# Kernel tuning notes

Measured on AMD Instinct MI355X. Metric: run time of the kernel, lower is better.

## Reference

```python
import jax, jax.numpy as jnp
import numpy as np

M = 28            # mask head resolution (mask_logit[i] is MxM)
NUM_CLASSES = 80  # max value of cls_idx (mask_image channel count)


def setup_inputs() -> dict:
    key = jax.random.key(0)
    k1, k2, k3, k4, k5, k6, k7 = jax.random.split(key, 7)
    N, H, W = 100, 800, 800
    cx = jax.random.uniform(k1, (N,), minval=0.0, maxval=float(W - 1))
    cy = jax.random.uniform(k2, (N,), minval=0.0, maxval=float(H - 1))
    bw = jax.random.uniform(k3, (N,), minval=20.0, maxval=300.0)
    bh = jax.random.uniform(k4, (N,), minval=20.0, maxval=300.0)
    mask_rois = jnp.stack([cx - bw / 2, cy - bh / 2, cx + bw / 2, cy + bh / 2], axis=1).astype(jnp.float32)
    cls_prob = jax.random.uniform(k5, (N,), dtype=jnp.float32)
    mask_prob = jax.random.normal(k6, (N, M, M), dtype=jnp.float32)
    cls_idx = jax.random.randint(k7, (N,), 1, NUM_CLASSES + 1, dtype=jnp.int32)
    return {"mask_rois": mask_rois, "cls_prob": cls_prob, "mask_prob": mask_prob,
            "cls_idx": cls_idx, "im_h": H, "im_w": W}


def _paste(logit, box, H, W):
    """Bilinear-paste an MxM logit into the full HxW image (== cv2.resize to (w,h)
    then placing at the box, evaluated directly on image pixel coords)."""
    x0, y0, x1, y1 = box[0], box[1], box[2], box[3]  # int32
    w = jnp.maximum(x1 - x0 + 1, 1).astype(jnp.float32)
    h = jnp.maximum(y1 - y0 + 1, 1).astype(jnp.float32)
    xs = jnp.arange(W, dtype=jnp.float32)
    ys = jnp.arange(H, dtype=jnp.float32)
    # cv2 bilinear mapping: src = (dst + 0.5) * (M / size) - 0.5, clamped at borders
    sx = jnp.clip((xs - x0.astype(jnp.float32) + 0.5) * (M / w) - 0.5, 0.0, M - 1.0)
    sy = jnp.clip((ys - y0.astype(jnp.float32) + 0.5) * (M / h) - 0.5, 0.0, M - 1.0)
    ix0 = jnp.floor(sx).astype(jnp.int32); ix1 = jnp.minimum(ix0 + 1, M - 1); fx = sx - ix0
    iy0 = jnp.floor(sy).astype(jnp.int32); iy1 = jnp.minimum(iy0 + 1, M - 1); fy = sy - iy0
    v00 = logit[iy0[:, None], ix0[None, :]]
    v01 = logit[iy0[:, None], ix1[None, :]]
    v10 = logit[iy1[:, None], ix0[None, :]]
    v11 = logit[iy1[:, None], ix1[None, :]]
    val = ((1 - fy)[:, None] * ((1 - fx)[None, :] * v00 + fx[None, :] * v01)
           + fy[:, None] * ((1 - fx)[None, :] * v10 + fx[None, :] * v11))
    xi = jnp.arange(W, dtype=jnp.int32)
    yi = jnp.arange(H, dtype=jnp.int32)
    inside_x = (xi >= jnp.maximum(x0, 0)) & (xi < jnp.minimum(x1 + 1, W))
    inside_y = (yi >= jnp.maximum(y0, 0)) & (yi < jnp.minimum(y1 + 1, H))
    inside = inside_y[:, None] & inside_x[None, :]
    return jnp.where(inside, val, 0.0), inside


def _forward(mask_rois, cls_prob, mask_prob, cls_idx, H, W, thr):
    N = mask_prob.shape[0]
    order = jnp.argsort(-cls_prob)                       # sort by score, descending
    boxes = mask_rois[order].astype(jnp.int32)
    logits = mask_prob[order]
    cls = cls_idx[order].astype(jnp.int32) - 1           # 0-based class ids
    pasted, inside = jax.vmap(lambda l, b: _paste(l, b, H, W))(logits, boxes)  # [N,H,W]

    def step(mask_image, xs):
        logit, ins, c = xs
        mask = (logit > 0) & ins                          # thresholded, in-image crop mask
        prev = mask_image[c]
        msum = jnp.sum(mask).astype(jnp.float32)
        ovl = jnp.sum(mask & prev).astype(jnp.float32)    # overlap with accumulated class mask
        keep = (msum > 0) & (ovl <= thr * msum)           # skip if ratio > threshold
        mask_image = mask_image.at[c].set(prev | (mask & keep))
        return mask_image, keep

    mask_image0 = jnp.zeros((NUM_CLASSES, H, W), dtype=bool)
    _, keep = jax.lax.scan(step, mask_image0, (pasted, inside, cls))

    # compact kept masks to the front (frame_id order); dropped boxes go to slot N (discarded)
    pos = jnp.where(keep, jnp.cumsum(keep.astype(jnp.int32)) - 1, N)
    energy = jnp.where(inside & keep[:, None, None], pasted, 0.0)
    full = jnp.zeros((N + 1, H, W), pasted.dtype).at[pos].set(energy)
    mask_energy = full[:N][None]                          # [1, N, H, W], kept masks first
    keep_inds = jnp.full((N + 1,), -1, jnp.int32).at[pos].set(
        jnp.where(keep, order.astype(jnp.int32), -1))[:N]
    return keep_inds, mask_energy


def reference(mask_rois, cls_prob, mask_prob, cls_idx, im_h, im_w):
    return _forward(mask_rois, cls_prob, mask_prob, cls_idx, int(im_h), int(im_w), 0.3)
```

## Files before the change

### kernel.cpp

```cpp
#include <hip/hip_runtime.h>

#define NINST 100
#define MLOG 28
#define IMG 800
#define LOGSZ (MLOG * MLOG)

#define OFF_ORDER 0
#define OFF_CLS   100
#define OFF_BOX   200
#define OFF_MSUM  600
#define OFF_SLOT  800
#define OFF_NK    900
#define OFF_NPAIR 901
#define OFF_FLAG  904
#define OFF_MASK  1024
#define ROWW      12
#define MSTRIDE   (ROWW * 304)
#define OFF_PAIRS (OFF_MASK + NINST * MSTRIDE)
#define PAIR_CAP  512
#define SLOTSZ    (IMG * IMG)
#define SUBB      40
#define ROWSPB    (IMG / SUBB)
#define MEGAGRID  (1 + NINST * SUBB)

__global__ __launch_bounds__(256) void k_raster(const float* __restrict__ mask_prob,
                                                const float* __restrict__ cls_prob,
                                                const float* __restrict__ rois,
                                                const int* __restrict__ cls_idx,
                                                int* __restrict__ ws) {
    int b = blockIdx.x, tid = threadIdx.x;
    __shared__ float s_p[NINST];
    __shared__ int s_order[NINST];
    __shared__ float lg[LOGSZ];
    __shared__ int red[256];
    if (tid < NINST) s_p[tid] = cls_prob[tid];
    __syncthreads();
    if (tid < NINST) {
        float p = s_p[tid];
        int r = 0;
        for (int j = 0; j < NINST; j++) {
            float q = s_p[j];
            r += (q > p) || (q == p && j < tid);
        }
        s_order[r] = tid;
    }
    __syncthreads();
    int n = b;
    int orig = s_order[n];
    int x0 = (int)rois[4 * orig], y0 = (int)rois[4 * orig + 1];
    int x1 = (int)rois[4 * orig + 2], y1 = (int)rois[4 * orig + 3];
    if (b == 0) {
        if (tid < NINST) {
            int o = s_order[tid];
            ws[OFF_ORDER + tid] = o;
            ws[OFF_CLS + tid] = cls_idx[o] - 1;
#pragma unroll
            for (int k = 0; k < 4; k++)
                ws[OFF_BOX + 4 * tid + k] = (int)rois[4 * o + k];
        }
    }
    for (int i = tid; i < LOGSZ; i += 256) lg[i] = mask_prob[orig * LOGSZ + i];
    __syncthreads();
    int xs = max(x0, 0), xe = min(x1 + 1, IMG);
    int ys = max(y0, 0), ye = min(y1 + 1, IMG);
    int wx0 = xs >> 5, nw = ((xe + 31) >> 5) - wx0, nrows = ye - ys;
    float wf = fmaxf((float)(x1 - x0 + 1), 1.f), hf = fmaxf((float)(y1 - y0 + 1), 1.f);
    float rx = 28.f / wf, ry = 28.f / hf;
    unsigned* mb = (unsigned*)(ws + OFF_MASK) + n * MSTRIDE;
    int total = nrows * nw, cnt = 0;
    for (int t = tid; t < total; t += 256) {
        int row = t / nw, wc = t - row * nw;
        int y = ys + row;
        float sy = ((float)y - (float)y0 + 0.5f) * ry - 0.5f;
        sy = fminf(fmaxf(sy, 0.f), 27.f);
        int iy0 = (int)sy, iy1 = min(iy0 + 1, 27);
        float fy = sy - (float)iy0;
        const float* r0 = lg + iy0 * MLOG;
        const float* r1 = lg + iy1 * MLOG;
        unsigned bits = 0u;
        int xbase = (wx0 + wc) << 5;
        int j0 = max(xs - xbase, 0), j1 = min(xe - xbase, 32);
        for (int j = j0; j < j1; j++) {
            int xx = xbase + j;
            float sx = ((float)xx - (float)x0 + 0.5f) * rx - 0.5f;
            sx = fminf(fmaxf(sx, 0.f), 27.f);
            int ix0 = (int)sx, ix1 = min(ix0 + 1, 27);
            float fx = sx - (float)ix0;
            float val = (1.f - fy) * ((1.f - fx) * r0[ix0] + fx * r0[ix1]) +
                        fy * ((1.f - fx) * r1[ix0] + fx * r1[ix1]);
            bits |= (val > 0.f) ? (1u << j) : 0u;
        }
        mb[row * ROWW + wc] = bits;
        cnt += __popc(bits);
    }
    red[tid] = cnt;
    __syncthreads();
    for (int s = 128; s; s >>= 1) {
        if (tid < s) red[tid] += red[tid + s];
        __syncthreads();
    }
    if (tid == 0) ws[OFF_MSUM + n] = red[0];
}

__global__ __launch_bounds__(256) void k_pairs(int* __restrict__ ws) {
    int b = blockIdx.x, tid = threadIdx.x;
    int wid = (b << 2) | (tid >> 6), lane = tid & 63;
    for (int idx = wid; idx < NINST * NINST; idx += (128 << 2)) {
        int i = idx / NINST, j = idx - i * NINST;
        if (i >= j) continue;
        if (ws[OFF_CLS + i] != ws[OFF_CLS + j]) continue;
        if (ws[OFF_MSUM + i] == 0 || ws[OFF_MSUM + j] == 0) continue;
        const int* bi = ws + OFF_BOX + 4 * i;
        const int* bj = ws + OFF_BOX + 4 * j;
        int ixs = max(bi[0], 0), ixe = min(bi[2] + 1, IMG);
        int iys = max(bi[1], 0), iye = min(bi[3] + 1, IMG);
        int jxs = max(bj[0], 0), jxe = min(bj[2] + 1, IMG);
        int jys = max(bj[1], 0), jye = min(bj[3] + 1, IMG);
        if (!(ixs < jxe && jxs < ixe && iys < jye && jys < iye)) continue;
        int iwx0 = ixs >> 5, jwx0 = jxs >> 5;
        int wlo = max(iwx0, jwx0);
        int whi = min((ixe + 31) >> 5, (jxe + 31) >> 5);
        int rlo = max(iys, jys), rhi = min(iye, jye);
        int nw = whi - wlo, nrows = rhi - rlo;
        const unsigned* mi = (const unsigned*)(ws + OFF_MASK) + i * MSTRIDE;
        const unsigned* mj = (const unsigned*)(ws + OFF_MASK) + j * MSTRIDE;
        int total = nrows * nw, cnt = 0;
        for (int t = lane; t < total; t += 64) {
            int row = t / nw, wc = t - row * nw;
            int y = rlo + row, w = wlo + wc;
            unsigned a = mi[(y - iys) * ROWW + (w - iwx0)];
            unsigned bb = mj[(y - jys) * ROWW + (w - jwx0)];
            cnt += __popc(a & bb);
        }
        for (int off = 32; off; off >>= 1) cnt += __shfl_down(cnt, off);
        if (lane == 0) {
            int k = atomicAdd(ws + OFF_NPAIR, 1);
            if (k < PAIR_CAP) {
                ws[OFF_PAIRS + 3 * k] = i;
                ws[OFF_PAIRS + 3 * k + 1] = j;
                ws[OFF_PAIRS + 3 * k + 2] = cnt;
            }
        }
    }
}

__global__ __launch_bounds__(256) void k_mega(const float* __restrict__ mask_prob,
                                              int* __restrict__ ws,
                                              float* __restrict__ out) {
    int b = blockIdx.x, tid = threadIdx.x;
    if (b > 0) {
        int s = (b - 1) / SUBB, sub = (b - 1) - s * SUBB;
        int r0 = sub * ROWSPB;
        float* base = out + NINST + (size_t)s * SLOTSZ + (size_t)r0 * IMG;
        float4* z = (float4*)base;
        for (int t = tid; t < (ROWSPB * IMG / 4); t += 256)
            z[t] = make_float4(0.f, 0.f, 0.f, 0.f);
        __syncthreads();
        if (tid == 0) {
            while (__hip_atomic_load(ws + OFF_FLAG, __ATOMIC_RELAXED,
                                     __HIP_MEMORY_SCOPE_AGENT) == 0)
                __builtin_amdgcn_s_sleep(32);
            __builtin_amdgcn_fence(__ATOMIC_ACQUIRE, "agent");
        }
        __syncthreads();
        int nk = ws[OFF_NK];
        if (s >= nk) return;
        int n = ws[OFF_SLOT + s];
        const int* box = ws + OFF_BOX + 4 * n;
        int x0 = box[0], y0 = box[1], x1 = box[2], y1 = box[3];
        int xs = max(x0, 0), xe = min(x1 + 1, IMG);
        int ys = max(y0, 0), ye = min(y1 + 1, IMG);
        int ya = max(ys, r0), yb = min(ye, r0 + ROWSPB);
        if (ya >= yb) return;
        __shared__ float lg[LOGSZ];
        int orig = ws[OFF_ORDER + n];
        for (int i = tid; i < LOGSZ; i += 256) lg[i] = mask_prob[orig * LOGSZ + i];
        __syncthreads();
        int xa = xs & ~3;
        int w4 = (xe - xa + 3) >> 2;
        int nrows = yb - ya, total = nrows * w4;
        float rx = 28.f / fmaxf((float)(x1 - x0 + 1), 1.f);
        float ry = 28.f / fmaxf((float)(y1 - y0 + 1), 1.f);
        float* sbase = out + NINST + (size_t)s * SLOTSZ;
        for (int t = tid; t < total; t += 256) {
            int row = t / w4, c4 = t - row * w4;
            int y = ya + row, xb = xa + (c4 << 2);
            float sy = ((float)y - (float)y0 + 0.5f) * ry - 0.5f;
            sy = fminf(fmaxf(sy, 0.f), 27.f);
            int iy0 = (int)sy, iy1 = min(iy0 + 1, 27);
            float fy = sy - (float)iy0;
            const float* rr0 = lg + iy0 * MLOG;
            const float* rr1 = lg + iy1 * MLOG;
            float vq[4];
#pragma unroll
            for (int j = 0; j < 4; j++) {
                int xx = xb + j;
                float val = 0.f;
                if (xx >= xs && xx < xe) {
                    float sx = ((float)xx - (float)x0 + 0.5f) * rx - 0.5f;
                    sx = fminf(fmaxf(sx, 0.f), 27.f);
                    int ix0 = (int)sx, ix1 = min(ix0 + 1, 27);
                    float fx = sx - (float)ix0;
                    val = (1.f - fy) * ((1.f - fx) * rr0[ix0] + fx * rr0[ix1]) +
                          fy * ((1.f - fx) * rr1[ix0] + fx * rr1[ix1]);
                }
                vq[j] = val;
            }
            *(float4*)(sbase + (size_t)y * IMG + xb) = make_float4(vq[0], vq[1], vq[2], vq[3]);
        }
        return;
    }
    __shared__ int s_box[4 * NINST];
    __shared__ int s_msum[NINST];
    __shared__ int s_keep[NINST];
    __shared__ int s_cand[32];
    __shared__ int s_ncand, s_sum, s_max, s_need;
    __shared__ int s_pi[PAIR_CAP], s_pj[PAIR_CAP], s_po[PAIR_CAP];
    __shared__ int red[256];
    for (int i = tid; i < NINST; i += 256) s_msum[i] = ws[OFF_MSUM + i];
    for (int i = tid; i < 4 * NINST; i += 256) s_box[i] = ws[OFF_BOX + i];
    int npair = min(ws[OFF_NPAIR], PAIR_CAP);
    for (int i = tid; i < npair; i += 256) {
        s_pi[i] = ws[OFF_PAIRS + 3 * i];
        s_pj[i] = ws[OFF_PAIRS + 3 * i + 1];
        s_po[i] = ws[OFF_PAIRS + 3 * i + 2];
    }
    const unsigned* maskbase = (const unsigned*)(ws + OFF_MASK);
    __syncthreads();
    for (int n = 0; n < NINST; n++) {
        if (tid == 0) { s_ncand = 0; s_sum = 0; s_max = 0; }
        __syncthreads();
        for (int q = tid; q < npair; q += 256) {
            if (s_pj[q] == n && s_keep[s_pi[q]]) {
                int k = atomicAdd(&s_ncand, 1);
                if (k < 32) s_cand[k] = s_pi[q];
                atomicAdd(&s_sum, s_po[q]);
                atomicMax(&s_max, s_po[q]);
            }
        }
        __syncthreads();
        if (tid == 0) {
            int msum = s_msum[n];
            float t = 0.3f * (float)msum;
            int keep, need = 0;
            if (s_ncand == 0 || (float)s_sum <= t) keep = (msum > 0);
            else if ((float)s_max > t) keep = 0;
            else { keep = 0; need = 1; }
            s_keep[n] = keep;
            s_need = need;
        }
        __syncthreads();
        if (s_need) {
            int nc = min(s_ncand, 32);
            int nxs = max(s_box[4 * n], 0), nxe = min(s_box[4 * n + 2] + 1, IMG);
            int nys = max(s_box[4 * n + 1], 0), nye = min(s_box[4 * n + 3] + 1, IMG);
            int wx0 = nxs >> 5, nw = ((nxe + 31) >> 5) - wx0, nrows = nye - nys;
            const unsigned* mn = maskbase + n * MSTRIDE;
            int total = nrows * nw, ovl = 0;
            for (int t2 = tid; t2 < total; t2 += 256) {
                int row = t2 / nw, wc = t2 - row * nw;
                unsigned bits = mn[row * ROWW + wc];
                if (!bits) continue;
                int y = nys + row, wa = wx0 + wc;
                unsigned img = 0;
                for (int k = 0; k < nc; k++) {
                    int m = s_cand[k];
                    int mys = max(s_box[4 * m + 1], 0), mye = min(s_box[4 * m + 3] + 1, IMG);
                    int mxs = max(s_box[4 * m], 0), mxe = min(s_box[4 * m + 2] + 1, IMG);
                    int mwx0 = mxs >> 5, mnw = ((mxe + 31) >> 5) - mwx0;
                    int rr = y - mys, cc = wa - mwx0;
                    if (rr >= 0 && rr < (mye - mys) && cc >= 0 && cc < mnw)
                        img |= maskbase[m * MSTRIDE + rr * ROWW + cc];
                }
                ovl += __popc(bits & img);
            }
            red[tid] = ovl;
            __syncthreads();
            for (int s = 128; s; s >>= 1) {
                if (tid < s) red[tid] += red[tid + s];
                __syncthreads();
            }
            if (tid == 0) {
                int msum = s_msum[n];
                s_keep[n] = (msum > 0) && ((float)red[0] <= 0.3f * (float)msum);
            }
        }
    }
    __syncthreads();
    if (tid == 0) {
        int nk = 0;
        for (int n = 0; n < NINST; n++) {
            if (s_keep[n]) {
                ws[OFF_SLOT + nk] = n;
                out[nk] = (float)ws[OFF_ORDER + n];
                nk++;
            }
        }
        ws[OFF_NK] = nk;
        for (int s = nk; s < NINST; s++) out[s] = -1.f;
        __builtin_amdgcn_fence(__ATOMIC_RELEASE, "agent");
        __hip_atomic_store(ws + OFF_FLAG, 1, __ATOMIC_RELAXED,
                           __HIP_MEMORY_SCOPE_AGENT);
    }
}

extern "C" void kernel_launch(void* const* d_in, const int* in_sizes, int n_in,
                              void* d_out, int out_size, void* d_ws, size_t ws_size,
                              hipStream_t stream) {
    const float* rois      = (const float*)d_in[0];
    const float* cls_prob  = (const float*)d_in[1];
    const float* mask_prob = (const float*)d_in[2];
    const int*   cls_idx   = (const int*)d_in[3];
    int* ws = (int*)d_ws;
    float* out = (float*)d_out;

    hipMemsetAsync(ws + OFF_NK, 0, 8 * sizeof(int), stream);
    k_raster<<<dim3(NINST), dim3(256), 0, stream>>>(mask_prob, cls_prob, rois, cls_idx, ws);
    k_pairs<<<dim3(128), dim3(256), 0, stream>>>(ws);
    k_mega<<<dim3(MEGAGRID), dim3(256), 0, stream>>>(mask_prob, ws, out);
}
```

Before: 357.8 us.

## Fold pair-overlap kernel into mega kernel's control block and drop memset

Removes the separate k_pairs launch and the hipMemsetAsync. Block 0 of k_mega now enumerates same-class overlapping pairs in shared memory and computes their bit-overlap counts itself. The sequential keep/drop scan runs in a single wavefront, with keep bits held in registers and shuffle/ballot reductions in place of block-wide syncs. The flag reset moves into k_raster, SUBB halves so each fill block zeroes more rows, and the spin sleep is shortened. The trade-off is that pair work is no longer spread over many blocks, so the serial control block may become longer while the fill blocks wait on it.

```diff
diff --git a/kernel.cpp b/kernel.cpp
--- a/kernel.cpp
+++ b/kernel.cpp
@@ -11,15 +11,13 @@
 #define OFF_MSUM  600
 #define OFF_SLOT  800
 #define OFF_NK    900
-#define OFF_NPAIR 901
 #define OFF_FLAG  904
 #define OFF_MASK  1024
 #define ROWW      12
 #define MSTRIDE   (ROWW * 304)
-#define OFF_PAIRS (OFF_MASK + NINST * MSTRIDE)
 #define PAIR_CAP  512
 #define SLOTSZ    (IMG * IMG)
-#define SUBB      40
+#define SUBB      20
 #define ROWSPB    (IMG / SUBB)
 #define MEGAGRID  (1 + NINST * SUBB)
 
@@ -50,6 +48,7 @@
     int x0 = (int)rois[4 * orig], y0 = (int)rois[4 * orig + 1];
     int x1 = (int)rois[4 * orig + 2], y1 = (int)rois[4 * orig + 3];
     if (b == 0) {
+        if (tid == 0) ws[OFF_FLAG] = 0;
         if (tid < NINST) {
             int o = s_order[tid];
             ws[OFF_ORDER + tid] = o;
@@ -102,64 +101,22 @@
     if (tid == 0) ws[OFF_MSUM + n] = red[0];
 }
 
-__global__ __launch_bounds__(256) void k_pairs(int* __restrict__ ws) {
+__global__ __launch_bounds__(256, 8) void k_mega(const float* __restrict__ mask_prob,
+                                                 int* __restrict__ ws,
+                                                 float* __restrict__ out) {
     int b = blockIdx.x, tid = threadIdx.x;
-    int wid = (b << 2) | (tid >> 6), lane = tid & 63;
-    for (int idx = wid; idx < NINST * NINST; idx += (128 << 2)) {
-        int i = idx / NINST, j = idx - i * NINST;
-        if (i >= j) continue;
-        if (ws[OFF_CLS + i] != ws[OFF_CLS + j]) continue;
-        if (ws[OFF_MSUM + i] == 0 || ws[OFF_MSUM + j] == 0) continue;
-        const int* bi = ws + OFF_BOX + 4 * i;
-        const int* bj = ws + OFF_BOX + 4 * j;
-        int ixs = max(bi[0], 0), ixe = min(bi[2] + 1, IMG);
-        int iys = max(bi[1], 0), iye = min(bi[3] + 1, IMG);
-        int jxs = max(bj[0], 0), jxe = min(bj[2] + 1, IMG);
-        int jys = max(bj[1], 0), jye = min(bj[3] + 1, IMG);
-        if (!(ixs < jxe && jxs < ixe && iys < jye && jys < iye)) continue;
-        int iwx0 = ixs >> 5, jwx0 = jxs >> 5;
-        int wlo = max(iwx0, jwx0);
-        int whi = min((ixe + 31) >> 5, (jxe + 31) >> 5);
-        int rlo = max(iys, jys), rhi = min(iye, jye);
-        int nw = whi - wlo, nrows = rhi - rlo;
-        const unsigned* mi = (const unsigned*)(ws + OFF_MASK) + i * MSTRIDE;
-        const unsigned* mj = (const unsigned*)(ws + OFF_MASK) + j * MSTRIDE;
-        int total = nrows * nw, cnt = 0;
-        for (int t = lane; t < total; t += 64) {
-            int row = t / nw, wc = t - row * nw;
-            int y = rlo + row, w = wlo + wc;
-            unsigned a = mi[(y - iys) * ROWW + (w - iwx0)];
-            unsigned bb = mj[(y - jys) * ROWW + (w - jwx0)];
-            cnt += __popc(a & bb);
-        }
-        for (int off = 32; off; off >>= 1) cnt += __shfl_down(cnt, off);
-        if (lane == 0) {
-            int k = atomicAdd(ws + OFF_NPAIR, 1);
-            if (k < PAIR_CAP) {
-                ws[OFF_PAIRS + 3 * k] = i;
-                ws[OFF_PAIRS + 3 * k + 1] = j;
-                ws[OFF_PAIRS + 3 * k + 2] = cnt;
-            }
-        }
-    }
-}
-
-__global__ __launch_bounds__(256) void k_mega(const float* __restrict__ mask_prob,
-                                              int* __restrict__ ws,
-                                              float* __restrict__ out) {
-    int b = blockIdx.x, tid = threadIdx.x;
+    const unsigned* maskbase = (const unsigned*)(ws + OFF_MASK);
     if (b > 0) {
         int s = (b - 1) / SUBB, sub = (b - 1) - s * SUBB;
         int r0 = sub * ROWSPB;
-        float* base = out + NINST + (size_t)s * SLOTSZ + (size_t)r0 * IMG;
-        float4* z = (float4*)base;
+        float4* z = (float4*)(out + NINST + (size_t)s * SLOTSZ + (size_t)r0 * IMG);
         for (int t = tid; t < (ROWSPB * IMG / 4); t += 256)
             z[t] = make_float4(0.f, 0.f, 0.f, 0.f);
         __syncthreads();
         if (tid == 0) {
             while (__hip_atomic_load(ws + OFF_FLAG, __ATOMIC_RELAXED,
                                      __HIP_MEMORY_SCOPE_AGENT) == 0)
-                __builtin_amdgcn_s_sleep(32);
+                __builtin_amdgcn_s_sleep(16);
             __builtin_amdgcn_fence(__ATOMIC_ACQUIRE, "agent");
         }
         __syncthreads();
@@ -178,7 +135,7 @@
         __syncthreads();
         int xa = xs & ~3;
         int w4 = (xe - xa + 3) >> 2;
-        int nrows = yb - ya, total = nrows * w4;
+        int total = (yb - ya) * w4;
         float rx = 28.f / fmaxf((float)(x1 - x0 + 1), 1.f);
         float ry = 28.f / fmaxf((float)(y1 - y0 + 1), 1.f);
         float* sbase = out + NINST + (size_t)s * SLOTSZ;
@@ -210,94 +167,136 @@
         }
         return;
     }
-    __shared__ int s_box[4 * NINST];
-    __shared__ int s_msum[NINST];
-    __shared__ int s_keep[NINST];
+    __shared__ int s_cls[NINST], s_msum[NINST], s_box[4 * NINST];
+    __shared__ int s_wi[PAIR_CAP], s_wj[PAIR_CAP], s_po[PAIR_CAP];
+    __shared__ int s_nw;
     __shared__ int s_cand[32];
-    __shared__ int s_ncand, s_sum, s_max, s_need;
-    __shared__ int s_pi[PAIR_CAP], s_pj[PAIR_CAP], s_po[PAIR_CAP];
-    __shared__ int red[256];
-    for (int i = tid; i < NINST; i += 256) s_msum[i] = ws[OFF_MSUM + i];
+    for (int i = tid; i < NINST; i += 256) {
+        s_cls[i] = ws[OFF_CLS + i];
+        s_msum[i] = ws[OFF_MSUM + i];
+    }
     for (int i = tid; i < 4 * NINST; i += 256) s_box[i] = ws[OFF_BOX + i];
-    int npair = min(ws[OFF_NPAIR], PAIR_CAP);
-    for (int i = tid; i < npair; i += 256) {
-        s_pi[i] = ws[OFF_PAIRS + 3 * i];
-        s_pj[i] = ws[OFF_PAIRS + 3 * i + 1];
-        s_po[i] = ws[OFF_PAIRS + 3 * i + 2];
-    }
-    const unsigned* maskbase = (const unsigned*)(ws + OFF_MASK);
-    __syncthreads();
+    if (tid == 0) s_nw = 0;
+    __syncthreads();
+    for (int c = tid; c < NINST * NINST; c += 256) {
+        int i = c / NINST, j = c - i * NINST;
+        if (i >= j) continue;
+        if (s_cls[i] != s_cls[j]) continue;
+        if (s_msum[i] == 0 || s_msum[j] == 0) continue;
+        int ixs = max(s_box[4 * i], 0), ixe = min(s_box[4 * i + 2] + 1, IMG);
+        int iys = max(s_box[4 * i + 1], 0), iye = min(s_box[4 * i + 3] + 1, IMG);
+        int jxs = max(s_box[4 * j], 0), jxe = min(s_box[4 * j + 2] + 1, IMG);
+        int jys = max(s_box[4 * j + 1], 0), jye = min(s_box[4 * j + 3] + 1, IMG);
+        if (!(ixs < jxe && jxs < ixe && iys < jye && jys < iye)) continue;
+        int k = atomicAdd(&s_nw, 1);
+        if (k < PAIR_CAP) { s_wi[k] = i; s_wj[k] = j; }
+    }
+    __syncthreads();
+    int nw = min(s_nw, PAIR_CAP);
+    int wid = tid >> 6, lane = tid & 63;
+    for (int k = wid; k < nw; k += 4) {
+        int i = s_wi[k], j = s_wj[k];
+        int ixs = max(s_box[4 * i], 0), ixe = min(s_box[4 * i + 2] + 1, IMG);
+        int iys = max(s_box[4 * i + 1], 0), iye = min(s_box[4 * i + 3] + 1, IMG);
+        int jxs = max(s_box[4 * j], 0), jxe = min(s_box[4 * j + 2] + 1, IMG);
+        int jys = max(s_box[4 * j + 1], 0);
+        int iwx0 = ixs >> 5, jwx0 = jxs >> 5;
+        int wlo = max(iwx0, jwx0);
+        int whi = min((ixe + 31) >> 5, (jxe + 31) >> 5);
+        int rlo = max(iys, jys);
+        int rhi = min(iye, min(s_box[4 * j + 3] + 1, IMG));
+        int nwrd = whi - wlo, nrows = rhi - rlo;
+        const unsigned* mi = maskbase + i * MSTRIDE;
+        const unsigned* mj = maskbase + j * MSTRIDE;
+        int total = nrows * nwrd, cnt = 0;
+        for (int t = lane; t < total; t += 64) {
+            int row = t / nwrd, wc = t - row * nwrd;
+            int y = rlo + row, w = wlo + wc;
+            unsigned a = mi[(y - iys) * ROWW + (w - iwx0)];
+            unsigned bb = mj[(y - jys) * ROWW + (w - jwx0)];
+            cnt += __popc(a & bb);
+        }
+        for (int off = 32; off; off >>= 1) cnt += __shfl_down(cnt, off);
+        if (lane == 0) s_po[k] = cnt;
+    }
+    __syncthreads();
+    if (tid >= 64) return;
+    unsigned long long k0 = 0, k1 = 0;
     for (int n = 0; n < NINST; n++) {
-        if (tid == 0) { s_ncand = 0; s_sum = 0; s_max = 0; }
-        __syncthreads();
-        for (int q = tid; q < npair; q += 256) {
-            if (s_pj[q] == n && s_keep[s_pi[q]]) {
-                int k = atomicAdd(&s_ncand, 1);
-                if (k < 32) s_cand[k] = s_pi[q];
-                atomicAdd(&s_sum, s_po[q]);
-                atomicMax(&s_max, s_po[q]);
-            }
-        }
-        __syncthreads();
-        if (tid == 0) {
-            int msum = s_msum[n];
-            float t = 0.3f * (float)msum;
-            int keep, need = 0;
-            if (s_ncand == 0 || (float)s_sum <= t) keep = (msum > 0);
-            else if ((float)s_max > t) keep = 0;
-            else { keep = 0; need = 1; }
-            s_keep[n] = keep;
-            s_need = need;
-        }
-        __syncthreads();
-        if (s_need) {
-            int nc = min(s_ncand, 32);
+        int msum = s_msum[n];
+        int lsum = 0, lmax = 0, lcnt = 0;
+        for (int q = lane; q < nw; q += 64) {
+            if (s_wj[q] == n) {
+                int pi = s_wi[q];
+                bool kb = (pi < 64) ? ((k0 >> pi) & 1ull) : ((k1 >> (pi - 64)) & 1ull);
+                if (kb) { int o = s_po[q]; lsum += o; lmax = max(lmax, o); lcnt++; }
+            }
+        }
+        for (int off = 32; off; off >>= 1) {
+            lsum += __shfl_xor(lsum, off);
+            lmax = max(lmax, __shfl_xor(lmax, off));
+            lcnt += __shfl_xor(lcnt, off);
+        }
+        float thr = 0.3f * (float)msum;
+        int keep;
+        if (lcnt == 0 || (float)lsum <= thr) keep = (msum > 0);
+        else if ((float)lmax > thr) keep = 0;
+        else {
+            int nc = 0;
+            for (int q0 = 0; q0 < nw; q0 += 64) {
+                int q = q0 + lane;
+                bool p = false; int piv = 0;
+                if (q < nw && s_wj[q] == n) {
+                    piv = s_wi[q];
+                    p = (piv < 64) ? ((k0 >> piv) & 1ull) : ((k1 >> (piv - 64)) & 1ull);
+                }
+                unsigned long long m = __ballot(p);
+                int pos = nc + __popcll(m & ((1ull << lane) - 1ull));
+                if (p && pos < 32) s_cand[pos] = piv;
+                nc += __popcll(m);
+            }
+            nc = min(nc, 32);
+            asm volatile("s_waitcnt lgkmcnt(0)" ::: "memory");
+            __builtin_amdgcn_sched_barrier(0);
             int nxs = max(s_box[4 * n], 0), nxe = min(s_box[4 * n + 2] + 1, IMG);
             int nys = max(s_box[4 * n + 1], 0), nye = min(s_box[4 * n + 3] + 1, IMG);
-            int wx0 = nxs >> 5, nw = ((nxe + 31) >> 5) - wx0, nrows = nye - nys;
+            int wx0 = nxs >> 5, nwrd = ((nxe + 31) >> 5) - wx0, nrows = nye - nys;
             const unsigned* mn = maskbase + n * MSTRIDE;
-            int total = nrows * nw, ovl = 0;
-            for (int t2 = tid; t2 < total; t2 += 256) {
-                int row = t2 / nw, wc = t2 - row * nw;
+            int total = nrows * nwrd, ovl = 0;
+            for (int t2 = lane; t2 < total; t2 += 64) {
+                int row = t2 / nwrd, wc = t2 - row * nwrd;
                 unsigned bits = mn[row * ROWW + wc];
                 if (!bits) continue;
                 int y = nys + row, wa = wx0 + wc;
                 unsigned img = 0;
                 for (int k = 0; k < nc; k++) {
-                    int m = s_cand[k];
-                    int mys = max(s_box[4 * m + 1], 0), mye = min(s_box[4 * m + 3] + 1, IMG);
-                    int mxs = max(s_box[4 * m], 0), mxe = min(s_box[4 * m + 2] + 1, IMG);
+                    int m2 = s_cand[k];
+                    int mys = max(s_box[4 * m2 + 1], 0), mye = min(s_box[4 * m2 + 3] + 1, IMG);
+                    int mxs = max(s_box[4 * m2], 0), mxe = min(s_box[4 * m2 + 2] + 1, IMG);
                     int mwx0 = mxs >> 5, mnw = ((mxe + 31) >> 5) - mwx0;
                     int rr = y - mys, cc = wa - mwx0;
                     if (rr >= 0 && rr < (mye - mys) && cc >= 0 && cc < mnw)
-                        img |= maskbase[m * MSTRIDE + rr * ROWW + cc];
+                        img |= maskbase[m2 * MSTRIDE + rr * ROWW + cc];
                 }
                 ovl += __popc(bits & img);
             }
-            red[tid] = ovl;
-            __syncthreads();
-            for (int s = 128; s; s >>= 1) {
-                if (tid < s) red[tid] += red[tid + s];
-                __syncthreads();
-            }
-            if (tid == 0) {
-                int msum = s_msum[n];
-                s_keep[n] = (msum > 0) && ((float)red[0] <= 0.3f * (float)msum);
-            }
-        }
-    }
-    __syncthreads();
-    if (tid == 0) {
+            for (int off = 32; off; off >>= 1) ovl += __shfl_xor(ovl, off);
+            keep = (msum > 0) && ((float)ovl <= thr);
+        }
+        if (keep) { if (n < 64) k0 |= 1ull << n; else k1 |= 1ull << (n - 64); }
+    }
+    if (lane == 0) {
         int nk = 0;
         for (int n = 0; n < NINST; n++) {
-            if (s_keep[n]) {
+            bool kb = (n < 64) ? ((k0 >> n) & 1ull) : ((k1 >> (n - 64)) & 1ull);
+            if (kb) {
                 ws[OFF_SLOT + nk] = n;
                 out[nk] = (float)ws[OFF_ORDER + n];
                 nk++;
             }
         }
         ws[OFF_NK] = nk;
-        for (int s = nk; s < NINST; s++) out[s] = -1.f;
+        for (int s2 = nk; s2 < NINST; s2++) out[s2] = -1.f;
         __builtin_amdgcn_fence(__ATOMIC_RELEASE, "agent");
         __hip_atomic_store(ws + OFF_FLAG, 1, __ATOMIC_RELAXED,
                            __HIP_MEMORY_SCOPE_AGENT);
@@ -314,8 +313,6 @@
     int* ws = (int*)d_ws;
     float* out = (float*)d_out;
 
-    hipMemsetAsync(ws + OFF_NK, 0, 8 * sizeof(int), stream);
     k_raster<<<dim3(NINST), dim3(256), 0, stream>>>(mask_prob, cls_prob, rois, cls_idx, ws);
-    k_pairs<<<dim3(128), dim3(256), 0, stream>>>(ws);
     k_mega<<<dim3(MEGAGRID), dim3(256), 0, stream>>>(mask_prob, ws, out);
 }
```

Result: slower. 376.9 us (+5.3%).
